# Kernel optimization log

Hardware: AMD Instinct MI355X
Metric: run time of the kernel (lower is better)

## Reference

```python
import jax, jax.numpy as jnp
import numpy as np

B, T, U, V = 8, 512, 128, 128  # batch, frames, label len (U+1 pred steps), vocab incl. blank
BLANK = 0


def setup_inputs() -> dict:
    key = jax.random.key(0)
    k1, k2, k3, k4 = jax.random.split(key, 4)
    logits = jax.random.normal(k1, (B, T, U + 1, V), dtype=jnp.float32)
    y = jax.random.randint(k2, (B, U), 1, V).astype(jnp.int32)  # labels, never blank
    logit_lens = jax.random.randint(k3, (B,), T // 2, T + 1).astype(jnp.int32)
    y_lens = jax.random.randint(k4, (B,), U // 2, U + 1).astype(jnp.int32)
    batch_offset = jnp.cumsum(logit_lens * (y_lens + 1)).astype(jnp.int32)
    return {
        "logits": logits,
        "y": y,
        "logit_lens": logit_lens,
        "y_lens": y_lens,
        "batch_offset": batch_offset,
        "max_f_len": T,
    }


def _combine(e1, e2):
    # log-domain affine recurrence x[u] = logaddexp(x[u-1] + c[u], a[u])
    c1, a1 = e1
    c2, a2 = e2
    return (c1 + c2, jnp.logaddexp(a1 + c2, a2))


def rnnt_loss(logits, y, logit_lens, y_lens, blank_idx):
    Bb, Tt, U1, Vv = logits.shape
    Uu = U1 - 1
    lp = jax.nn.log_softmax(logits, axis=-1)            # [B,T,U+1,V]
    blank = lp[..., blank_idx]                          # [B,T,U+1]
    idx = jnp.broadcast_to(y[:, None, :, None], (Bb, Tt, Uu, 1)).astype(jnp.int32)
    emit = jnp.take_along_axis(lp[:, :, :Uu, :], idx, axis=3)[..., 0]  # [B,T,U]

    # alpha[0,u] = sum_{v<u} emit(0,v)
    row0 = jnp.concatenate(
        [jnp.zeros((Bb, 1), lp.dtype), jnp.cumsum(emit[:, 0, :], axis=1)], axis=1
    )  # [B,U+1]
    neg = jnp.full((Bb, 1), -jnp.inf, lp.dtype)

    def step(prev_row, x):
        bl_prev, em_t = x                               # [B,U+1], [B,U]
        a = prev_row + bl_prev                          # come-from-below (blank at t-1)
        c = jnp.concatenate([neg, em_t], axis=1)        # come-from-left (emit at t)
        _, row = jax.lax.associative_scan(_combine, (c, a), axis=1)
        return row, row

    xs = (jnp.swapaxes(blank[:, : Tt - 1, :], 0, 1), jnp.swapaxes(emit[:, 1:, :], 0, 1))
    _, rows = jax.lax.scan(step, row0, xs)              # [T-1,B,U+1]
    alphas = jnp.swapaxes(jnp.concatenate([row0[None], rows], axis=0), 0, 1)  # [B,T,U+1]

    bi = jnp.arange(Bb)
    ti = logit_lens - 1
    ui = y_lens
    ll = alphas[bi, ti, ui] + blank[bi, ti, ui]
    return -ll                                          # per-utterance negative log-lik


def reference(logits, y, logit_lens, y_lens, batch_offset, max_f_len):
    # batch_offset / max_f_len are packing metadata, unused when packed_input=False
    return rnnt_loss(logits, y, logit_lens, y_lens, BLANK).mean()
```

## Files before the change

kernel.cpp:

```cpp
#include <hip/hip_runtime.h>

#define Bb 8
#define Tt 512
#define Uu 128
#define U1 129
#define Vv 128

#define OUT_OFF 0
#define CTROWS 321
#define PCKROW 512
#define PCKBSZ ((size_t)CTROWS * PCKROW)
#define PCK_OFF ((size_t)Bb * Tt * U1 * 2)
#define CTCOL_OFF (PCK_OFF + (size_t)Bb * PCKBSZ)
#define WROWF 768
#define WROWS 160
#define WBSZ ((size_t)WROWS * WROWF)
#define W_OFF (CTCOL_OFF + (size_t)Bb * CTROWS * 4)
#define WCOL_OFF (W_OFF + (size_t)Bb * WBSZ)
#define RES_OFF (WCOL_OFF + (size_t)Bb * WROWS * 8)

#define K_LN2    0.6931471805599453f
#define K_INVLN2 1.4426950408889634f
#define SENT (-1.0e30f)

__device__ __forceinline__ float fexp2(float x) {
    float r; asm("v_exp_f32 %0, %1" : "=v"(r) : "v"(x)); return r;
}
__device__ __forceinline__ float flog2(float x) {
    float r; asm("v_log_f32 %0, %1" : "=v"(r) : "v"(x)); return r;
}
__device__ __forceinline__ float fmax3(float x, float y, float z) {
    float r; asm("v_max3_f32 %0, %1, %2, %3" : "=v"(r) : "v"(x), "v"(y), "v"(z));
    return r;
}

__global__ __launch_bounds__(256) void lse_kernel(
    const float* __restrict__ logits, const int* __restrict__ y,
    const int* __restrict__ logit_lens, const int* __restrict__ y_lens,
    float* __restrict__ ws)
{
    const int b = blockIdx.y;
    const int t = blockIdx.x;
    if (t >= logit_lens[b]) return;
    const int Ue = y_lens[b];

    float2* outv = (float2*)(ws + OUT_OFF);
    const int wid  = threadIdx.x >> 6;
    const int lane = threadIdx.x & 63;
    const int g    = lane >> 4;
    const int gl   = lane & 15;
    const unsigned rowbase = ((unsigned)b * Tt + t) * U1;
    const int yb = b * Uu;

    for (int u0 = wid * 8; u0 <= Ue; u0 += 32) {
        const int ua = u0 + g;
        const int ub = u0 + 4 + g;
        const int uca = ua > Ue ? Ue : ua;
        const int ucb = ub > Ue ? Ue : ub;
        const float* pa = logits + (size_t)(rowbase + uca) * Vv;
        const float* pb = logits + (size_t)(rowbase + ucb) * Vv;
        float4 a1 = *(const float4*)(pa + gl * 4);
        float4 a2 = *(const float4*)(pa + 64 + gl * 4);
        float4 b1 = *(const float4*)(pb + gl * 4);
        float4 b2 = *(const float4*)(pb + 64 + gl * 4);

        float sa = (fexp2(a1.x * K_INVLN2) + fexp2(a1.y * K_INVLN2))
                 + (fexp2(a1.z * K_INVLN2) + fexp2(a1.w * K_INVLN2))
                 + (fexp2(a2.x * K_INVLN2) + fexp2(a2.y * K_INVLN2))
                 + (fexp2(a2.z * K_INVLN2) + fexp2(a2.w * K_INVLN2));
        float sb = (fexp2(b1.x * K_INVLN2) + fexp2(b1.y * K_INVLN2))
                 + (fexp2(b1.z * K_INVLN2) + fexp2(b1.w * K_INVLN2))
                 + (fexp2(b2.x * K_INVLN2) + fexp2(b2.y * K_INVLN2))
                 + (fexp2(b2.z * K_INVLN2) + fexp2(b2.w * K_INVLN2));
        #pragma unroll
        for (int off = 8; off; off >>= 1) {
            sa += __shfl_xor(sa, off);
            sb += __shfl_xor(sb, off);
        }
        float lseA = flog2(sa);
        float lseB = flog2(sb);

        float emA = SENT, emB = SENT;
        if (uca < Uu) {
            int yv = y[yb + uca];
            int c = yv & 3;
            float4 cv = (yv & 64) ? a2 : a1;
            float cand = (c == 0) ? cv.x : (c == 1) ? cv.y : (c == 2) ? cv.z : cv.w;
            float ev = __shfl(cand, (lane & 48) | ((yv & 63) >> 2));
            emA = ev * K_INVLN2 - lseA;
        }
        if (ucb < Uu) {
            int yv = y[yb + ucb];
            int c = yv & 3;
            float4 cv = (yv & 64) ? b2 : b1;
            float cand = (c == 0) ? cv.x : (c == 1) ? cv.y : (c == 2) ? cv.z : cv.w;
            float ev = __shfl(cand, (lane & 48) | ((yv & 63) >> 2));
            emB = ev * K_INVLN2 - lseB;
        }
        if (gl == 0) {
            if (ua <= Ue) outv[rowbase + ua] = make_float2(a1.x * K_INVLN2 - lseA, emA);
            if (ub <= Ue) outv[rowbase + ub] = make_float2(b1.x * K_INVLN2 - lseB, emB);
        }
    }
}

__device__ __forceinline__ float lae2(float x, float y) {
    float dd = x - y;
    float nad = __builtin_bit_cast(float, __builtin_bit_cast(int, dd) | 0x80000000);
    return fmaxf(x, y) + flog2(1.0f + fexp2(nad));
}
__device__ __forceinline__ float lae3(float x, float y, float z) {
    float m = fmax3(x, y, z);
    return m + flog2(fexp2(x - m) + fexp2(y - m) + fexp2(z - m));
}
__device__ __forceinline__ float lae5(float a, float b, float c, float d, float e) {
    float m = fmax3(a, b, c);
    m = fmax3(m, d, e);
    return m + flog2(fexp2(a - m) + fexp2(b - m) + fexp2(c - m)
                   + fexp2(d - m) + fexp2(e - m));
}

__global__ __launch_bounds__(256) void cond_kernel(
    const int* __restrict__ logit_lens, const int* __restrict__ y_lens,
    float* __restrict__ ws)
{
    const int b = blockIdx.x / 320;
    const int m = blockIdx.x - b * 320 + 1;
    if (m > ((logit_lens[b] - 1 + y_lens[b]) >> 1)) return;
    const int r1 = 2 * m - 2, r2 = 2 * m - 1;
    const float2* outv = (const float2*)(ws + OUT_OFF);

    __shared__ float2 D1[U1], D2[U1];
    __shared__ float pckS[PCKROW];
    for (int q = threadIdx.x; q < 2 * U1; q += 256) {
        const int which = q >= U1;
        const int j = q - which * U1;
        const int t = (which ? r2 : r1) - j;
        float2 val = make_float2(SENT, SENT);
        if (t >= 0 && t < Tt) val = outv[((size_t)b * Tt + t) * U1 + j];
        (which ? D2 : D1)[j] = val;
    }
    __syncthreads();

    const int u = threadIdx.x;
    if (u <= 128) {
        float2 d1  = D1[u], d2 = D2[u];
        float2 d1m = (u >= 1) ? D1[u - 1] : make_float2(SENT, SENT);
        float d2my  = (u >= 1) ? D2[u - 1].y : SENT;
        float d1m2y = (u >= 2) ? D1[u - 2].y : SENT;
        float A = d1.x + d2.x;
        float B = lae2(d1m.y + d2.x, d1m.x + d2my);
        float C = d1m2y + d2my;
        if (u < 128) {
            int base = (u >> 1) * 8 + (u & 1);
            pckS[base]     = A;
            pckS[base + 2] = B;
            pckS[base + 4] = C;
            if ((u & 1) == 0) { pckS[base + 6] = 0.0f; pckS[base + 7] = 0.0f; }
        } else {
            ((float4*)(ws + CTCOL_OFF))[(size_t)b * CTROWS + m] = make_float4(A, B, C, 0.0f);
        }
    }
    __syncthreads();

    float* pckG = ws + PCK_OFF + (size_t)b * PCKBSZ + (size_t)m * PCKROW;
    for (int i = threadIdx.x; i < PCKROW; i += 256) pckG[i] = pckS[i];
}

__global__ __launch_bounds__(256) void compose_kernel(
    const int* __restrict__ logit_lens, const int* __restrict__ y_lens,
    float* __restrict__ ws)
{
    const int b = blockIdx.x / 159;
    const int q = blockIdx.x - b * 159 + 1;
    const int dend = logit_lens[b] - 1 + y_lens[b];
    if (4 * q > dend) return;
    const int m1 = 2 * q - 1, m2 = 2 * q;
    const float* PCKb = ws + PCK_OFF + (size_t)b * PCKBSZ;
    const float4* COLb = (const float4*)(ws + CTCOL_OFF) + (size_t)b * CTROWS;

    __shared__ float a1s[131], b1s[131], c1s[131];
    __shared__ float wrk[WROWF];
    const int u = threadIdx.x;
    if (u < 2) { a1s[u] = SENT; b1s[u] = SENT; c1s[u] = SENT; }
    if (u < 128) {
        const float* p = PCKb + (size_t)m1 * PCKROW + (u >> 1) * 8;
        int par = u & 1;
        a1s[u + 2] = p[par]; b1s[u + 2] = p[2 + par]; c1s[u + 2] = p[4 + par];
    } else if (u == 128) {
        float4 cc = COLb[m1];
        a1s[130] = cc.x; b1s[130] = cc.y; c1s[130] = cc.z;
    }
    __syncthreads();

    if (u <= 128) {
        float A2, B2, C2;
        if (u < 128) {
            const float* p = PCKb + (size_t)m2 * PCKROW + (u >> 1) * 8;
            int par = u & 1;
            A2 = p[par]; B2 = p[2 + par]; C2 = p[4 + par];
        } else {
            float4 cc = COLb[m2];
            A2 = cc.x; B2 = cc.y; C2 = cc.z;
        }
        float A1 = a1s[u + 2], A1m = a1s[u + 1], A1m2 = a1s[u];
        float B1 = b1s[u + 2], B1m = b1s[u + 1], B1m2 = b1s[u];
        float C1 = c1s[u + 2], C1m = c1s[u + 1], C1m2 = c1s[u];
        float W0 = A2 + A1;
        float W1 = lae2(A2 + B1, B2 + A1m);
        float W2 = lae3(A2 + C1, B2 + B1m, C2 + A1m2);
        float W3 = lae2(B2 + C1m, C2 + B1m2);
        float W4 = C2 + C1m2;
        if (u < 128) {
            int base = (u >> 1) * 12 + (u & 1);
            wrk[base]     = W0;
            wrk[base + 2] = W1;
            wrk[base + 4] = W2;
            wrk[base + 6] = W3;
            wrk[base + 8] = W4;
            if ((u & 1) == 0) { wrk[base + 10] = 0.0f; wrk[base + 11] = 0.0f; }
        } else {
            float* wc = ws + WCOL_OFF + ((size_t)b * WROWS + q) * 8;
            wc[0] = W0; wc[1] = W1; wc[2] = W2; wc[3] = W3; wc[4] = W4;
            wc[5] = 0.0f; wc[6] = 0.0f; wc[7] = 0.0f;
        }
    }
    __syncthreads();

    float* wg = ws + W_OFF + (size_t)b * WBSZ + (size_t)q * WROWF;
    for (int i = threadIdx.x; i < WROWF; i += 256) wg[i] = wrk[i];
}

template<int MODE>
__device__ __forceinline__ float rot1(float x, int lane) {
    if constexpr (MODE == 2) {
        float s = __shfl_up(x, 1);
        float w = __shfl(x, 63);
        return (lane == 0) ? w : s;
    } else {
        constexpr int CTRL = (MODE == 0) ? 0x13C : 0x134;
        int i = __builtin_bit_cast(int, x);
        i = __builtin_amdgcn_update_dpp(i, i, CTRL, 0xF, 0xF, true);
        return __builtin_bit_cast(float, i);
    }
}

template<int MODE, bool H128>
__device__ __forceinline__ void dp_body(int b, int lane, int Tb, int Ub,
                                        float* __restrict__ ws)
{
    const float2* outv = (const float2*)(ws + OUT_OFF);
    const float* PCKb = ws + PCK_OFF + (size_t)b * PCKBSZ;
    const float4* COLb = (const float4*)(ws + CTCOL_OFF) + (size_t)b * CTROWS;
    const float* WTb = ws + W_OFF + (size_t)b * WBSZ;
    const float* WCb = ws + WCOL_OFF + (size_t)b * WROWS * 8;
    int zv; asm volatile("v_mov_b32 %0, 0" : "=v"(zv));

    float px = (lane == 0) ? 0.0f : SENT;
    float py = SENT, p2 = SENT;
    const int dend = Tb - 1 + Ub;
    const int nq   = dend >> 2;
    const int rem  = dend & 3;

    const int mpair = 2 * nq + 1;
    float4 Qp = *(const float4*)(PCKb + (size_t)mpair * PCKROW + (lane << 3));
    float2 Rp = *(const float2*)(PCKb + (size_t)mpair * PCKROW + (lane << 3) + 4);
    float4 Op = make_float4(SENT, SENT, SENT, 0.0f);
    if constexpr (H128) Op = COLb[mpair + zv];

    float2 F1 = make_float2(0,0), F2 = make_float2(0,0), G = make_float2(0,0);
    if (rem & 1) {
        const int r = dend - 1;
        int j1 = 2 * lane, j2 = 2 * lane + 1;
        int t1 = r - j1; t1 = t1 > Tt - 1 ? Tt - 1 : t1;
        int t2 = r - j2; t2 = t2 > Tt - 1 ? Tt - 1 : t2;
        F1 = outv[((size_t)b * Tt + t1) * U1 + j1];
        F2 = outv[((size_t)b * Tt + t2) * U1 + j2];
        if constexpr (H128) G = outv[((size_t)b * Tt + (r - 128)) * U1 + 128];
    }
    float pbf = outv[((size_t)b * Tt + (Tb - 1)) * U1 + Ub + zv].x;

    float4 A0,A1,A2,A3,A4,A5,A6,A7;
    float4 B0,B1,B2,B3,B4,B5,B6,B7;
    float2 C0,C1,C2,C3,C4,C5,C6,C7;
    float4 Oa0,Oa1,Oa2,Oa3,Oa4,Oa5,Oa6,Oa7;
    float2 Oc0,Oc1,Oc2,Oc3,Oc4,Oc5,Oc6,Oc7;

#define LOADW(i, qq) { unsigned o = (unsigned)(qq) * WROWF + lane * 12; \
    A##i = *(const float4*)(WTb + o); \
    B##i = *(const float4*)(WTb + o + 4); \
    C##i = *(const float2*)(WTb + o + 8); \
    if constexpr (H128) { \
        Oa##i = *(const float4*)(WCb + (qq) * 8 + zv); \
        Oc##i = *(const float2*)(WCb + (qq) * 8 + 4 + zv); } }

#define PIN(i) if constexpr (H128) { \
        asm volatile("" : "+v"(A##i.x), "+v"(A##i.y), "+v"(A##i.z), "+v"(A##i.w), \
                          "+v"(B##i.x), "+v"(B##i.y), "+v"(B##i.z), "+v"(B##i.w), \
                          "+v"(C##i.x), "+v"(C##i.y), \
                          "+v"(Oa##i.x), "+v"(Oa##i.y), "+v"(Oa##i.z), "+v"(Oa##i.w), \
                          "+v"(Oc##i.x)); \
    } else { \
        asm volatile("" : "+v"(A##i.x), "+v"(A##i.y), "+v"(A##i.z), "+v"(A##i.w), \
                          "+v"(B##i.x), "+v"(B##i.y), "+v"(B##i.z), "+v"(B##i.w), \
                          "+v"(C##i.x), "+v"(C##i.y)); \
    }

#define COMP4(i) { \
    float p1y = rot1<MODE>(py, lane); \
    float p1x = rot1<MODE>(px, lane); \
    float p2y = rot1<MODE>(p1y, lane); \
    float p2x = rot1<MODE>(p1x, lane); \
    float nx = lae5(px + A##i.x, p1y + A##i.z, p1x + B##i.x, p2y + B##i.z, p2x + C##i.x); \
    float ny = lae5(py + A##i.y, px + A##i.w, p1y + B##i.y, p1x + B##i.w, p2y + C##i.y); \
    if constexpr (H128) p2 = lae5(p2 + Oa##i.x, p1y + Oa##i.y, p1x + Oa##i.z, \
                                  p2y + Oa##i.w, p2x + Oc##i.x); \
    px = nx; py = ny; }

    LOADW(0,1) LOADW(1,2) LOADW(2,3) LOADW(3,4)
    LOADW(4,5) LOADW(5,6) LOADW(6,7) LOADW(7,8)

    int q = 1;
    for (; q + 7 <= nq; q += 8) {
        PIN(0) COMP4(0) { int dn = q + 8  > nq ? nq : q + 8;  LOADW(0, dn) }
        PIN(1) COMP4(1) { int dn = q + 9  > nq ? nq : q + 9;  LOADW(1, dn) }
        PIN(2) COMP4(2) { int dn = q + 10 > nq ? nq : q + 10; LOADW(2, dn) }
        PIN(3) COMP4(3) { int dn = q + 11 > nq ? nq : q + 11; LOADW(3, dn) }
        PIN(4) COMP4(4) { int dn = q + 12 > nq ? nq : q + 12; LOADW(4, dn) }
        PIN(5) COMP4(5) { int dn = q + 13 > nq ? nq : q + 13; LOADW(5, dn) }
        PIN(6) COMP4(6) { int dn = q + 14 > nq ? nq : q + 14; LOADW(6, dn) }
        PIN(7) COMP4(7) { int dn = q + 15 > nq ? nq : q + 15; LOADW(7, dn) }
    }
#define TAILW(i) if (q <= nq) { PIN(i) COMP4(i) q++; }
    TAILW(0) TAILW(1) TAILW(2) TAILW(3) TAILW(4) TAILW(5) TAILW(6)

    if (rem >= 2) {
        float pm1 = rot1<MODE>(py, lane);
        float pm0 = rot1<MODE>(px, lane);
        float nx = lae3(px + Qp.x, pm1 + Qp.z, pm0 + Rp.x);
        float ny = lae3(py + Qp.y, px + Qp.w, pm1 + Rp.y);
        if constexpr (H128) p2 = lae3(p2 + Op.x, pm1 + Op.y, pm0 + Op.z);
        px = nx; py = ny;
    }
    if (rem & 1) {
        float pm  = rot1<MODE>(py, lane);
        float pmE = rot1<MODE>(F2.y, lane);
        float pmE0 = (lane == 0) ? SENT : pmE;
        float nx = lae2(px + F1.x, pm + pmE0);
        float ny = lae2(py + F2.x, px + F1.y);
        if constexpr (H128) p2 = lae2(p2 + G.x, pm + pmE);
        px = nx; py = ny;
    }

    float a;
    if constexpr (H128) {
        a = __shfl(p2, 0);
    } else {
        float ax = __shfl(px, Ub >> 1);
        float ay = __shfl(py, Ub >> 1);
        a = (Ub & 1) ? ay : ax;
    }
    if (lane == 0) {
        ws[RES_OFF + b] = -(a + pbf) * K_LN2;
    }
#undef LOADW
#undef PIN
#undef COMP4
#undef TAILW
}

__global__ __launch_bounds__(64) void dp_kernel(
    const int* __restrict__ logit_lens, const int* __restrict__ y_lens,
    float* __restrict__ ws)
{
    const int b = blockIdx.x;
    const int lane = threadIdx.x;
    const int Tb = logit_lens[b];
    const int Ub = y_lens[b];
    const bool h = (Ub == 128);
    int li = lane;
    int r0 = __builtin_amdgcn_update_dpp(li, li, 0x13C , 0xF, 0xF, true);
    int r1 = __builtin_amdgcn_update_dpp(li, li, 0x134 , 0xF, 0xF, true);
    int want = (lane + 63) & 63;
    if (__all(r0 == want)) {
        if (h) dp_body<0, true>(b, lane, Tb, Ub, ws);
        else   dp_body<0, false>(b, lane, Tb, Ub, ws);
    } else if (__all(r1 == want)) {
        if (h) dp_body<1, true>(b, lane, Tb, Ub, ws);
        else   dp_body<1, false>(b, lane, Tb, Ub, ws);
    } else {
        if (h) dp_body<2, true>(b, lane, Tb, Ub, ws);
        else   dp_body<2, false>(b, lane, Tb, Ub, ws);
    }
}

__global__ void mean_kernel(const float* __restrict__ res, float* __restrict__ out)
{
    if (threadIdx.x == 0) {
        float s = 0.0f;
        #pragma unroll
        for (int i = 0; i < Bb; ++i) s += res[i];
        out[0] = s * (1.0f / Bb);
    }
}

extern "C" void kernel_launch(void* const* d_in, const int* in_sizes, int n_in,
                              void* d_out, int out_size, void* d_ws, size_t ws_size,
                              hipStream_t stream) {
    const float* logits     = (const float*)d_in[0];
    const int*   y          = (const int*)d_in[1];
    const int*   logit_lens = (const int*)d_in[2];
    const int*   y_lens     = (const int*)d_in[3];
    float* ws  = (float*)d_ws;
    float* out = (float*)d_out;

    dim3 lgrid(Tt, Bb);
    lse_kernel<<<lgrid, 256, 0, stream>>>(logits, y, logit_lens, y_lens, ws);
    cond_kernel<<<Bb * 320, 256, 0, stream>>>(logit_lens, y_lens, ws);
    compose_kernel<<<Bb * 159, 256, 0, stream>>>(logit_lens, y_lens, ws);
    dp_kernel<<<Bb, 64, 0, stream>>>(logit_lens, y_lens, ws);
    mean_kernel<<<1, 64, 0, stream>>>(ws + RES_OFF, out);
}
```

Before: 68.73 us.

## Split serial RNNT DP into meet-in-the-middle forward and backward passes

The sequential per-batch alpha recurrence over composed 4-diagonal transition blocks is split in two. One wavefront runs forward over the first half of the diagonals and a second runs a transposed backward (beta-style) recurrence over the second half. A new combine kernel joins the two frontiers with a log-sum-exp reduction. compose_kernel now also writes a transposed weight layout for the backward pass. This targets the latency of the single-wave serial chain, which dominates. The cost is twice the DP wavefronts, extra workspace writes in compose, and one more kernel launch.

Result: faster. 64.54 us (-6.1%).

```diff
diff --git a/kernel.cpp b/kernel.cpp
--- a/kernel.cpp
+++ b/kernel.cpp
@@ -17,7 +17,9 @@
 #define WBSZ ((size_t)WROWS * WROWF)
 #define W_OFF (CTCOL_OFF + (size_t)Bb * CTROWS * 4)
 #define WCOL_OFF (W_OFF + (size_t)Bb * WBSZ)
-#define RES_OFF (WCOL_OFF + (size_t)Bb * WROWS * 8)
+#define WB_OFF (WCOL_OFF + (size_t)Bb * WROWS * 8)
+#define ST_OFF (WB_OFF + (size_t)Bb * WBSZ)
+#define RES_OFF (ST_OFF + (size_t)Bb * 260)
 
 #define K_LN2    0.6931471805599453f
 #define K_INVLN2 1.4426950408889634f
@@ -32,6 +34,26 @@
 __device__ __forceinline__ float fmax3(float x, float y, float z) {
     float r; asm("v_max3_f32 %0, %1, %2, %3" : "=v"(r) : "v"(x), "v"(y), "v"(z));
     return r;
+}
+__device__ __forceinline__ float lae2(float x, float y) {
+    float dd = x - y;
+    float nad = __builtin_bit_cast(float, __builtin_bit_cast(int, dd) | 0x80000000);
+    return fmaxf(x, y) + flog2(1.0f + fexp2(nad));
+}
+__device__ __forceinline__ float lae3(float x, float y, float z) {
+    float m = fmax3(x, y, z);
+    return m + flog2(fexp2(x - m) + fexp2(y - m) + fexp2(z - m));
+}
+__device__ __forceinline__ float lae5(float a, float b, float c, float d, float e) {
+    float m = fmax3(a, b, c);
+    m = fmax3(m, d, e);
+    return m + flog2(fexp2(a - m) + fexp2(b - m) + fexp2(c - m)
+                   + fexp2(d - m) + fexp2(e - m));
+}
+__device__ __forceinline__ float lae6(float a, float b, float c, float d, float e, float f) {
+    float m = fmaxf(fmax3(a, b, c), fmax3(d, e, f));
+    return m + flog2(fexp2(a - m) + fexp2(b - m) + fexp2(c - m)
+                   + fexp2(d - m) + fexp2(e - m) + fexp2(f - m));
 }
 
 __global__ __launch_bounds__(256) void lse_kernel(
@@ -102,22 +124,6 @@
             if (ub <= Ue) outv[rowbase + ub] = make_float2(b1.x * K_INVLN2 - lseB, emB);
         }
     }
-}
-
-__device__ __forceinline__ float lae2(float x, float y) {
-    float dd = x - y;
-    float nad = __builtin_bit_cast(float, __builtin_bit_cast(int, dd) | 0x80000000);
-    return fmaxf(x, y) + flog2(1.0f + fexp2(nad));
-}
-__device__ __forceinline__ float lae3(float x, float y, float z) {
-    float m = fmax3(x, y, z);
-    return m + flog2(fexp2(x - m) + fexp2(y - m) + fexp2(z - m));
-}
-__device__ __forceinline__ float lae5(float a, float b, float c, float d, float e) {
-    float m = fmax3(a, b, c);
-    m = fmax3(m, d, e);
-    return m + flog2(fexp2(a - m) + fexp2(b - m) + fexp2(c - m)
-                   + fexp2(d - m) + fexp2(e - m));
 }
 
 __global__ __launch_bounds__(256) void cond_kernel(
@@ -180,7 +186,8 @@
     const float4* COLb = (const float4*)(ws + CTCOL_OFF) + (size_t)b * CTROWS;
 
     __shared__ float a1s[131], b1s[131], c1s[131];
-    __shared__ float wrk[WROWF];
+    __shared__ float wrk[WROWF], wrkB[WROWF];
+    __shared__ float sW0[129], sW1[129], sW2[129], sW3[129], sW4[129];
     const int u = threadIdx.x;
     if (u < 2) { a1s[u] = SENT; b1s[u] = SENT; c1s[u] = SENT; }
     if (u < 128) {
@@ -211,6 +218,7 @@
         float W2 = lae3(A2 + C1, B2 + B1m, C2 + A1m2);
         float W3 = lae2(B2 + C1m, C2 + B1m2);
         float W4 = C2 + C1m2;
+        sW0[u] = W0; sW1[u] = W1; sW2[u] = W2; sW3[u] = W3; sW4[u] = W4;
         if (u < 128) {
             int base = (u >> 1) * 12 + (u & 1);
             wrk[base]     = W0;
@@ -227,16 +235,33 @@
     }
     __syncthreads();
 
-    float* wg = ws + W_OFF + (size_t)b * WBSZ + (size_t)q * WROWF;
-    for (int i = threadIdx.x; i < WROWF; i += 256) wg[i] = wrk[i];
+    if (u < 64) {
+        const int l = u, e = 2 * l;
+        float cx2 = (e + 2 <= 127) ? sW2[e + 2] : SENT;
+        float cx3 = (e + 3 <= 127) ? sW3[e + 3] : SENT;
+        float cx4 = (e + 4 <= 127) ? sW4[e + 4] : SENT;
+        float cy1 = (e + 2 <= 127) ? sW1[e + 2] : SENT;
+        float cy2 = (e + 3 <= 127) ? sW2[e + 3] : SENT;
+        float cy3 = (e + 4 <= 127) ? sW3[e + 4] : SENT;
+        float cy4 = (e + 5 <= 127) ? sW4[e + 5] : SENT;
+        float c5x = (l == 62) ? sW4[128] : (l == 63) ? sW2[128] : SENT;
+        float c5y = (l == 62) ? sW3[128] : (l == 63) ? sW1[128] : SENT;
+        float* rb = wrkB + l * 12;
+        rb[0] = sW0[e];     rb[1] = sW1[e + 1]; rb[2]  = cx2; rb[3]  = cx3;
+        rb[4] = cx4;        rb[5] = sW0[e + 1]; rb[6]  = cy1; rb[7]  = cy2;
+        rb[8] = cy3;        rb[9] = cy4;        rb[10] = c5x; rb[11] = c5y;
+    }
+    __syncthreads();
+
+    float* wg  = ws + W_OFF  + (size_t)b * WBSZ + (size_t)q * WROWF;
+    float* wbg = ws + WB_OFF + (size_t)b * WBSZ + (size_t)q * WROWF;
+    for (int i = threadIdx.x; i < WROWF; i += 256) { wg[i] = wrk[i]; wbg[i] = wrkB[i]; }
 }
 
 template<int MODE>
-__device__ __forceinline__ float rot1(float x, int lane) {
+__device__ __forceinline__ float rotU(float x, int lane) {
     if constexpr (MODE == 2) {
-        float s = __shfl_up(x, 1);
-        float w = __shfl(x, 63);
-        return (lane == 0) ? w : s;
+        return __shfl(x, (lane + 63) & 63);
     } else {
         constexpr int CTRL = (MODE == 0) ? 0x13C : 0x134;
         int i = __builtin_bit_cast(int, x);
@@ -244,14 +269,22 @@
         return __builtin_bit_cast(float, i);
     }
 }
+template<int MODE>
+__device__ __forceinline__ float rotD(float x, int lane) {
+    if constexpr (MODE == 2) {
+        return __shfl(x, (lane + 1) & 63);
+    } else {
+        constexpr int CTRL = (MODE == 0) ? 0x134 : 0x13C;
+        int i = __builtin_bit_cast(int, x);
+        i = __builtin_amdgcn_update_dpp(i, i, CTRL, 0xF, 0xF, true);
+        return __builtin_bit_cast(float, i);
+    }
+}
 
 template<int MODE, bool H128>
-__device__ __forceinline__ void dp_body(int b, int lane, int Tb, int Ub,
+__device__ __forceinline__ void fw_body(int b, int lane, int Tb, int Ub,
                                         float* __restrict__ ws)
 {
-    const float2* outv = (const float2*)(ws + OUT_OFF);
-    const float* PCKb = ws + PCK_OFF + (size_t)b * PCKBSZ;
-    const float4* COLb = (const float4*)(ws + CTCOL_OFF) + (size_t)b * CTROWS;
     const float* WTb = ws + W_OFF + (size_t)b * WBSZ;
     const float* WCb = ws + WCOL_OFF + (size_t)b * WROWS * 8;
     int zv; asm volatile("v_mov_b32 %0, 0" : "=v"(zv));
@@ -260,25 +293,7 @@
     float py = SENT, p2 = SENT;
     const int dend = Tb - 1 + Ub;
     const int nq   = dend >> 2;
-    const int rem  = dend & 3;
-
-    const int mpair = 2 * nq + 1;
-    float4 Qp = *(const float4*)(PCKb + (size_t)mpair * PCKROW + (lane << 3));
-    float2 Rp = *(const float2*)(PCKb + (size_t)mpair * PCKROW + (lane << 3) + 4);
-    float4 Op = make_float4(SENT, SENT, SENT, 0.0f);
-    if constexpr (H128) Op = COLb[mpair + zv];
-
-    float2 F1 = make_float2(0,0), F2 = make_float2(0,0), G = make_float2(0,0);
-    if (rem & 1) {
-        const int r = dend - 1;
-        int j1 = 2 * lane, j2 = 2 * lane + 1;
-        int t1 = r - j1; t1 = t1 > Tt - 1 ? Tt - 1 : t1;
-        int t2 = r - j2; t2 = t2 > Tt - 1 ? Tt - 1 : t2;
-        F1 = outv[((size_t)b * Tt + t1) * U1 + j1];
-        F2 = outv[((size_t)b * Tt + t2) * U1 + j2];
-        if constexpr (H128) G = outv[((size_t)b * Tt + (r - 128)) * U1 + 128];
-    }
-    float pbf = outv[((size_t)b * Tt + (Tb - 1)) * U1 + Ub + zv].x;
+    const int qend = nq >> 1;
 
     float4 A0,A1,A2,A3,A4,A5,A6,A7;
     float4 B0,B1,B2,B3,B4,B5,B6,B7;
@@ -307,10 +322,10 @@
     }
 
 #define COMP4(i) { \
-    float p1y = rot1<MODE>(py, lane); \
-    float p1x = rot1<MODE>(px, lane); \
-    float p2y = rot1<MODE>(p1y, lane); \
-    float p2x = rot1<MODE>(p1x, lane); \
+    float p1y = rotU<MODE>(py, lane); \
+    float p1x = rotU<MODE>(px, lane); \
+    float p2y = rotU<MODE>(p1y, lane); \
+    float p2x = rotU<MODE>(p1x, lane); \
     float nx = lae5(px + A##i.x, p1y + A##i.z, p1x + B##i.x, p2y + B##i.z, p2x + C##i.x); \
     float ny = lae5(py + A##i.y, px + A##i.w, p1y + B##i.y, p1x + B##i.w, p2y + C##i.y); \
     if constexpr (H128) p2 = lae5(p2 + Oa##i.x, p1y + Oa##i.y, p1x + Oa##i.z, \
@@ -321,77 +336,185 @@
     LOADW(4,5) LOADW(5,6) LOADW(6,7) LOADW(7,8)
 
     int q = 1;
-    for (; q + 7 <= nq; q += 8) {
-        PIN(0) COMP4(0) { int dn = q + 8  > nq ? nq : q + 8;  LOADW(0, dn) }
-        PIN(1) COMP4(1) { int dn = q + 9  > nq ? nq : q + 9;  LOADW(1, dn) }
-        PIN(2) COMP4(2) { int dn = q + 10 > nq ? nq : q + 10; LOADW(2, dn) }
-        PIN(3) COMP4(3) { int dn = q + 11 > nq ? nq : q + 11; LOADW(3, dn) }
-        PIN(4) COMP4(4) { int dn = q + 12 > nq ? nq : q + 12; LOADW(4, dn) }
-        PIN(5) COMP4(5) { int dn = q + 13 > nq ? nq : q + 13; LOADW(5, dn) }
-        PIN(6) COMP4(6) { int dn = q + 14 > nq ? nq : q + 14; LOADW(6, dn) }
-        PIN(7) COMP4(7) { int dn = q + 15 > nq ? nq : q + 15; LOADW(7, dn) }
-    }
-#define TAILW(i) if (q <= nq) { PIN(i) COMP4(i) q++; }
+    for (; q + 7 <= qend; q += 8) {
+        PIN(0) COMP4(0) { int dn = q + 8  > qend ? qend : q + 8;  LOADW(0, dn) }
+        PIN(1) COMP4(1) { int dn = q + 9  > qend ? qend : q + 9;  LOADW(1, dn) }
+        PIN(2) COMP4(2) { int dn = q + 10 > qend ? qend : q + 10; LOADW(2, dn) }
+        PIN(3) COMP4(3) { int dn = q + 11 > qend ? qend : q + 11; LOADW(3, dn) }
+        PIN(4) COMP4(4) { int dn = q + 12 > qend ? qend : q + 12; LOADW(4, dn) }
+        PIN(5) COMP4(5) { int dn = q + 13 > qend ? qend : q + 13; LOADW(5, dn) }
+        PIN(6) COMP4(6) { int dn = q + 14 > qend ? qend : q + 14; LOADW(6, dn) }
+        PIN(7) COMP4(7) { int dn = q + 15 > qend ? qend : q + 15; LOADW(7, dn) }
+    }
+#define TAILW(i) if (q <= qend) { PIN(i) COMP4(i) q++; }
     TAILW(0) TAILW(1) TAILW(2) TAILW(3) TAILW(4) TAILW(5) TAILW(6)
 
-    if (rem >= 2) {
-        float pm1 = rot1<MODE>(py, lane);
-        float pm0 = rot1<MODE>(px, lane);
-        float nx = lae3(px + Qp.x, pm1 + Qp.z, pm0 + Rp.x);
-        float ny = lae3(py + Qp.y, px + Qp.w, pm1 + Rp.y);
-        if constexpr (H128) p2 = lae3(p2 + Op.x, pm1 + Op.y, pm0 + Op.z);
-        px = nx; py = ny;
-    }
-    if (rem & 1) {
-        float pm  = rot1<MODE>(py, lane);
-        float pmE = rot1<MODE>(F2.y, lane);
-        float pmE0 = (lane == 0) ? SENT : pmE;
-        float nx = lae2(px + F1.x, pm + pmE0);
-        float ny = lae2(py + F2.x, px + F1.y);
-        if constexpr (H128) p2 = lae2(p2 + G.x, pm + pmE);
-        px = nx; py = ny;
-    }
-
-    float a;
-    if constexpr (H128) {
-        a = __shfl(p2, 0);
-    } else {
-        float ax = __shfl(px, Ub >> 1);
-        float ay = __shfl(py, Ub >> 1);
-        a = (Ub & 1) ? ay : ax;
-    }
-    if (lane == 0) {
-        ws[RES_OFF + b] = -(a + pbf) * K_LN2;
-    }
+    float* F = ws + ST_OFF + (size_t)b * 260;
+    ((float2*)F)[lane] = make_float2(px, py);
+    if (lane == 0) F[128] = H128 ? p2 : SENT;
 #undef LOADW
 #undef PIN
 #undef COMP4
 #undef TAILW
 }
 
+template<int MODE>
+__device__ __forceinline__ void bw_body(int b, int lane, int Tb, int Ub,
+                                        float* __restrict__ ws)
+{
+    const float2* outv = (const float2*)(ws + OUT_OFF);
+    const float* PCKb = ws + PCK_OFF + (size_t)b * PCKBSZ;
+    const float4* COLb = (const float4*)(ws + CTCOL_OFF) + (size_t)b * CTROWS;
+    const float* WBb = ws + WB_OFF + (size_t)b * WBSZ;
+    const float* WCb = ws + WCOL_OFF + (size_t)b * WROWS * 8;
+    int zv; asm volatile("v_mov_b32 %0, 0" : "=v"(zv));
+
+    const int dend = Tb - 1 + Ub;
+    const int nq   = dend >> 2;
+    const int qlo  = (nq >> 1) + 1;
+    const int rem  = dend & 3;
+
+    float wx = SENT, wy = SENT, w128 = SENT;
+    if (Ub == 128) w128 = 0.0f;
+    else if (lane == (Ub >> 1)) { if (Ub & 1) wy = 0.0f; else wx = 0.0f; }
+
+    float4 X0,X1,X2,X3,X4,X5,X6,X7;
+    float4 Y0,Y1,Y2,Y3,Y4,Y5,Y6,Y7;
+    float4 Z0,Z1,Z2,Z3,Z4,Z5,Z6,Z7;
+    float w0c0,w0c1,w0c2,w0c3,w0c4,w0c5,w0c6,w0c7;
+
+#define LOADB(i, qq) { unsigned o = (unsigned)(qq) * WROWF + lane * 12; \
+    X##i = *(const float4*)(WBb + o); \
+    Y##i = *(const float4*)(WBb + o + 4); \
+    Z##i = *(const float4*)(WBb + o + 8); \
+    w0c##i = *(WCb + (qq) * 8 + zv); }
+
+#define PINB(i) asm volatile("" : "+v"(X##i.x), "+v"(X##i.y), "+v"(X##i.z), "+v"(X##i.w), \
+                          "+v"(Y##i.x), "+v"(Y##i.y), "+v"(Y##i.z), "+v"(Y##i.w), \
+                          "+v"(Z##i.x), "+v"(Z##i.y), "+v"(Z##i.z), "+v"(Z##i.w), \
+                          "+v"(w0c##i));
+
+#define CLD(v) ((v) < qlo ? qlo : (v))
+    LOADB(0, CLD(nq))     LOADB(1, CLD(nq - 1)) LOADB(2, CLD(nq - 2)) LOADB(3, CLD(nq - 3))
+    LOADB(4, CLD(nq - 4)) LOADB(5, CLD(nq - 5)) LOADB(6, CLD(nq - 6)) LOADB(7, CLD(nq - 7))
+
+    if (rem & 1) {
+        const int r = dend - 1;
+        int j1 = 2 * lane, j2 = 2 * lane + 1;
+        int t1 = r - j1; t1 = t1 > Tt - 1 ? Tt - 1 : t1; if (t1 < 0) t1 = 0;
+        int t2 = r - j2; t2 = t2 > Tt - 1 ? Tt - 1 : t2; if (t2 < 0) t2 = 0;
+        float2 F1 = outv[((size_t)b * Tt + t1) * U1 + j1];
+        float2 F2 = outv[((size_t)b * Tt + t2) * U1 + j2];
+        int tg = r - 128; if (tg < 0) tg = 0;
+        float2 G = outv[((size_t)b * Tt + tg) * U1 + 128];
+        float n1x = rotD<MODE>(wx, lane);
+        float nx = lae2(F1.x + wx, F1.y + wy);
+        float ny = lae2(F2.x + wy, F2.y + ((lane == 63) ? w128 : n1x));
+        w128 = G.x + w128;
+        wx = nx; wy = ny;
+    }
+    if (rem >= 2) {
+        const int mpair = 2 * nq + 1;
+        const float* prow = PCKb + (size_t)mpair * PCKROW;
+        float4 Qp  = *(const float4*)(prow + (lane << 3));
+        float2 Rp  = *(const float2*)(prow + (lane << 3) + 4);
+        int lp = lane + 1 > 63 ? 63 : lane + 1;
+        float4 QpN = *(const float4*)(prow + (lp << 3));
+        float2 RpN = *(const float2*)(prow + (lp << 3) + 4);
+        float4 Op  = COLb[mpair + zv];
+        float n1x = rotD<MODE>(wx, lane), n1y = rotD<MODE>(wy, lane);
+        float nx = lae3(Qp.x + wx, Qp.w + wy,
+                        (lane == 63) ? (Op.z + w128) : (RpN.x + n1x));
+        float ny = lae3(Qp.y + wy,
+                        (lane == 63) ? (Op.y + w128) : (QpN.z + n1x),
+                        (lane == 63) ? SENT : (RpN.y + n1y));
+        w128 = Op.x + w128;
+        wx = nx; wy = ny;
+    }
+
+#define COMPB(i) { \
+    float n1x = rotD<MODE>(wx, lane), n1y = rotD<MODE>(wy, lane); \
+    float n2x = rotD<MODE>(n1x, lane), n2y = rotD<MODE>(n1y, lane); \
+    float nx = lae6(wx + X##i.x, wy + X##i.y, n1x + X##i.z, n1y + X##i.w, \
+                    n2x + Y##i.x, Z##i.z + w128); \
+    float ny = lae6(wy + Y##i.y, n1x + Y##i.z, n1y + Y##i.w, n2x + Z##i.x, \
+                    n2y + Z##i.y, Z##i.w + w128); \
+    w128 = w0c##i + w128; \
+    wx = nx; wy = ny; }
+
+    int q = nq;
+    for (; q - 7 >= qlo; q -= 8) {
+        PINB(0) COMPB(0) LOADB(0, CLD(q - 8))
+        PINB(1) COMPB(1) LOADB(1, CLD(q - 9))
+        PINB(2) COMPB(2) LOADB(2, CLD(q - 10))
+        PINB(3) COMPB(3) LOADB(3, CLD(q - 11))
+        PINB(4) COMPB(4) LOADB(4, CLD(q - 12))
+        PINB(5) COMPB(5) LOADB(5, CLD(q - 13))
+        PINB(6) COMPB(6) LOADB(6, CLD(q - 14))
+        PINB(7) COMPB(7) LOADB(7, CLD(q - 15))
+    }
+#define TAILB(i) if (q >= qlo) { PINB(i) COMPB(i) q--; }
+    TAILB(0) TAILB(1) TAILB(2) TAILB(3) TAILB(4) TAILB(5) TAILB(6)
+
+    float* Bst = ws + ST_OFF + (size_t)b * 260 + 130;
+    ((float2*)Bst)[lane] = make_float2(wx, wy);
+    if (lane == 0) Bst[128] = w128;
+#undef LOADB
+#undef PINB
+#undef CLD
+#undef COMPB
+#undef TAILB
+}
+
 __global__ __launch_bounds__(64) void dp_kernel(
     const int* __restrict__ logit_lens, const int* __restrict__ y_lens,
     float* __restrict__ ws)
 {
-    const int b = blockIdx.x;
+    const int b   = blockIdx.x >> 1;
+    const int dir = blockIdx.x & 1;
     const int lane = threadIdx.x;
     const int Tb = logit_lens[b];
     const int Ub = y_lens[b];
     const bool h = (Ub == 128);
     int li = lane;
-    int r0 = __builtin_amdgcn_update_dpp(li, li, 0x13C , 0xF, 0xF, true);
-    int r1 = __builtin_amdgcn_update_dpp(li, li, 0x134 , 0xF, 0xF, true);
-    int want = (lane + 63) & 63;
-    if (__all(r0 == want)) {
-        if (h) dp_body<0, true>(b, lane, Tb, Ub, ws);
-        else   dp_body<0, false>(b, lane, Tb, Ub, ws);
-    } else if (__all(r1 == want)) {
-        if (h) dp_body<1, true>(b, lane, Tb, Ub, ws);
-        else   dp_body<1, false>(b, lane, Tb, Ub, ws);
+    int r0 = __builtin_amdgcn_update_dpp(li, li, 0x13C, 0xF, 0xF, true);
+    int r1 = __builtin_amdgcn_update_dpp(li, li, 0x134, 0xF, 0xF, true);
+    int wantU = (lane + 63) & 63, wantD = (lane + 1) & 63;
+    int mode = 2;
+    if (__all(r0 == wantU) && __all(r1 == wantD)) mode = 0;
+    else if (__all(r1 == wantU) && __all(r0 == wantD)) mode = 1;
+
+    if (dir == 0) {
+        if (mode == 0)      { if (h) fw_body<0, true>(b, lane, Tb, Ub, ws); else fw_body<0, false>(b, lane, Tb, Ub, ws); }
+        else if (mode == 1) { if (h) fw_body<1, true>(b, lane, Tb, Ub, ws); else fw_body<1, false>(b, lane, Tb, Ub, ws); }
+        else                { if (h) fw_body<2, true>(b, lane, Tb, Ub, ws); else fw_body<2, false>(b, lane, Tb, Ub, ws); }
     } else {
-        if (h) dp_body<2, true>(b, lane, Tb, Ub, ws);
-        else   dp_body<2, false>(b, lane, Tb, Ub, ws);
-    }
+        if (mode == 0)      bw_body<0>(b, lane, Tb, Ub, ws);
+        else if (mode == 1) bw_body<1>(b, lane, Tb, Ub, ws);
+        else                bw_body<2>(b, lane, Tb, Ub, ws);
+    }
+}
+
+__global__ __launch_bounds__(64) void combine_kernel(
+    const int* __restrict__ logit_lens, const int* __restrict__ y_lens,
+    float* __restrict__ ws)
+{
+    const int b = blockIdx.x;
+    const int lane = threadIdx.x;
+    const float* F = ws + ST_OFF + (size_t)b * 260;
+    const float* Bs = F + 130;
+    float2 v = ((const float2*)F)[lane];
+    float2 w = ((const float2*)Bs)[lane];
+    float r = lae2(v.x + w.x, v.y + w.y);
+    #pragma unroll
+    for (int off = 32; off; off >>= 1)
+        r = lae2(r, __shfl_xor(r, off));
+    r = lae2(r, F[128] + Bs[128]);
+    const int Tb = logit_lens[b], Ub = y_lens[b];
+    const float2* outv = (const float2*)(ws + OUT_OFF);
+    float pbf = outv[((size_t)b * Tt + (Tb - 1)) * U1 + Ub].x;
+    if (lane == 0)
+        ws[RES_OFF + b] = -(r + pbf) * K_LN2;
 }
 
 __global__ void mean_kernel(const float* __restrict__ res, float* __restrict__ out)
@@ -418,6 +541,7 @@
     lse_kernel<<<lgrid, 256, 0, stream>>>(logits, y, logit_lens, y_lens, ws);
     cond_kernel<<<Bb * 320, 256, 0, stream>>>(logit_lens, y_lens, ws);
     compose_kernel<<<Bb * 159, 256, 0, stream>>>(logit_lens, y_lens, ws);
-    dp_kernel<<<Bb, 64, 0, stream>>>(logit_lens, y_lens, ws);
+    dp_kernel<<<Bb * 2, 64, 0, stream>>>(logit_lens, y_lens, ws);
+    combine_kernel<<<Bb, 64, 0, stream>>>(logit_lens, y_lens, ws);
     mean_kernel<<<1, 64, 0, stream>>>(ws + RES_OFF, out);
 }
```
